# Performance work log

Measured on AMD Instinct MI355X. Metric: run time of the kernel, lower is better.

The kernel has to match this reference:

```python
import jax, jax.numpy as jnp
import numpy as np

B, S, M, D, H, DH = 2, 1024, 1024, 1024, 16, 64
K = S + M                 # key length
R = 2 * K - 1             # relative position table width
EPS = 1e-5


def layer_norm(x, gamma, beta):
    mu = jnp.mean(x, axis=-1, keepdims=True)
    var = jnp.mean(jnp.square(x - mu), axis=-1, keepdims=True)
    return (x - mu) * jax.lax.rsqrt(var + EPS) * gamma + beta


def skew(q_pos, mem_len):
    # q_pos: (B, H, L, R) with R = 2*k_len - 1
    b, h, L, r = q_pos.shape
    pad = jnp.full((b, h, L, 1), -jnp.inf, q_pos.dtype)
    x = jnp.concatenate([q_pos, pad], axis=-1).reshape(b, h, L * (r + 1))
    x = x[..., : L * r].reshape(b, h, L, r)
    k_len = (r + 1) // 2
    start = k_len - 1 - mem_len
    return x[..., start : start + k_len]  # (B, H, L, k_len)


def setup_inputs() -> dict:
    key = jax.random.key(0)
    ks = jax.random.split(key, 9)
    hidden = jax.random.normal(ks[0], (B, S, D), jnp.float32)
    memory = jax.random.normal(ks[1], (B, M, D), jnp.float32)
    pos_emb = jax.random.normal(ks[2], (B, R, DH), jnp.float32)
    # causal mask: query i may attend keys j <= i + M ; True = blocked
    mask = jnp.arange(K)[None, :] > (jnp.arange(S)[:, None] + M)
    sc = 1.0 / np.sqrt(D)
    Wq = jax.random.normal(ks[3], (D, H * DH), jnp.float32) * sc
    Wk = jax.random.normal(ks[4], (D, H * DH), jnp.float32) * sc
    Wv = jax.random.normal(ks[5], (D, H * DH), jnp.float32) * sc
    Wo = jax.random.normal(ks[6], (H * DH, D), jnp.float32) * sc
    gamma = jnp.ones((D,), jnp.float32)
    beta = jnp.zeros((D,), jnp.float32)
    return {"hidden": hidden, "pos_emb": pos_emb, "memory": memory,
            "mask": mask, "Wq": Wq, "Wk": Wk, "Wv": Wv, "Wo": Wo,
            "gamma": gamma, "beta": beta}


def reference(hidden, pos_emb, memory, mask, Wq, Wk, Wv, Wo, gamma, beta):
    mem_len = memory.shape[1]
    combined = jnp.concatenate([memory, hidden], axis=1)  # (B, K, D)
    h_ln = layer_norm(hidden, gamma, beta)                # pre-LN
    c_ln = layer_norm(combined, gamma, beta)
    q = (h_ln @ Wq).reshape(B, S, H, DH).transpose(0, 2, 1, 3)  # (B,H,S,DH)
    k = (c_ln @ Wk).reshape(B, K, H, DH).transpose(0, 2, 1, 3)  # (B,H,K,DH)
    v = (c_ln @ Wv).reshape(B, K, H, DH).transpose(0, 2, 1, 3)
    score = jnp.einsum('bhsd,bhkd->bhsk', q, k)                  # (B,H,S,K)
    q_pos = jnp.einsum('bhsd,brd->bhsr', q, pos_emb)             # (B,H,S,R)
    score = (score + skew(q_pos, mem_len)) * (1.0 / np.sqrt(D))
    score = jnp.where(mask[None, None], -jnp.inf, score)
    p = jax.nn.softmax(score, axis=-1)
    attn = jnp.einsum('bhsk,bhkd->bshd', p, v).reshape(B, S, H * DH)
    out = attn @ Wo
    return h_ln + out
```

## Files before the change

### kernel.cpp

```cpp
#include <hip/hip_runtime.h>
#include <hip/hip_bf16.h>

#define B_ 2
#define S_ 1024
#define M_ 1024
#define D_ 1024
#define H_ 16
#define DH_ 64
#define K_ 2048
#define R_ 4095

#define NEG_BIG (-1e30f)

typedef unsigned short u16;
typedef short short8 __attribute__((ext_vector_type(8)));
typedef float f32x4 __attribute__((ext_vector_type(4)));

__device__ __forceinline__ u16 f2bf(float f) {
  __hip_bfloat16 h = __float2bfloat16(f);
  return *reinterpret_cast<u16*>(&h);
}
__device__ __forceinline__ float bf2f(u16 u) {
  __hip_bfloat16 h;
  *reinterpret_cast<u16*>(&h) = u;
  return __bfloat162float(h);
}

__device__ __forceinline__ void gll16(const void* g, const void* l) {
  __builtin_amdgcn_global_load_lds(
      (const __attribute__((address_space(1))) unsigned int*)g,
      (__attribute__((address_space(3))) unsigned int*)l, 16, 0, 0);
}

__device__ __forceinline__ f32x4 mfma16(short8 a, short8 b, f32x4 c) {
  return __builtin_amdgcn_mfma_f32_16x16x32_bf16(a, b, c, 0, 0, 0);
}

__global__ __launch_bounds__(256) void prep_kernel(
    const float* __restrict__ hidden, const float* __restrict__ memory,
    const float* __restrict__ gamma, const float* __restrict__ beta,
    u16* __restrict__ cln,
    const float* __restrict__ W0, const float* __restrict__ W1,
    const float* __restrict__ W2, const float* __restrict__ W3,
    u16* __restrict__ O0, u16* __restrict__ O1,
    u16* __restrict__ O2, u16* __restrict__ O3,
    const float* __restrict__ pos, u16* __restrict__ posb) {
  __shared__ u16 tile[64][66];
  __shared__ float red[8];
  const int bx = blockIdx.x;
  const int t = threadIdx.x;

  if (bx < 4096) {
    const int b = bx >> 11;
    const int idx = bx & (K_ - 1);
    const float* src = (idx < M_)
        ? memory + (size_t)(b * M_ + idx) * D_
        : hidden + (size_t)(b * S_ + (idx - M_)) * D_;
    const int lane = t & 63, w = t >> 6;
    float4 rv = ((const float4*)src)[t];
    float s = rv.x + rv.y + rv.z + rv.w;
    float ss = rv.x * rv.x + rv.y * rv.y + rv.z * rv.z + rv.w * rv.w;
#pragma unroll
    for (int m = 1; m < 64; m <<= 1) {
      s += __shfl_xor(s, m, 64);
      ss += __shfl_xor(ss, m, 64);
    }
    if (lane == 0) { red[w] = s; red[4 + w] = ss; }
    __syncthreads();
    s = red[0] + red[1] + red[2] + red[3];
    ss = red[4] + red[5] + red[6] + red[7];
    const float mu = s * (1.0f / D_);
    const float var = ss * (1.0f / D_) - mu * mu;
    const float rstd = rsqrtf(var + 1e-5f);
    float4 gv = ((const float4*)gamma)[t];
    float4 bv = ((const float4*)beta)[t];
    ushort4 ov;
    ov.x = f2bf((rv.x - mu) * rstd * gv.x + bv.x);
    ov.y = f2bf((rv.y - mu) * rstd * gv.y + bv.y);
    ov.z = f2bf((rv.z - mu) * rstd * gv.z + bv.z);
    ov.w = f2bf((rv.w - mu) * rstd * gv.w + bv.w);
    ((ushort4*)(cln + (size_t)bx * D_))[t] = ov;
    return;
  }
  if (bx < 5120) {
    const int z = (bx - 4096) >> 8;
    const int rem = (bx - 4096) & 255;
    const float* in; u16* out;
    switch (z) {
      case 0:  in = W0; out = O0; break;
      case 1:  in = W1; out = O1; break;
      case 2:  in = W2; out = O2; break;
      default: in = W3; out = O3; break;
    }
    const int tx = t & 63, ty = t >> 6;
    const int k0 = (rem & 15) * 64, n0 = (rem >> 4) * 64;
#pragma unroll
    for (int i = ty; i < 64; i += 4)
      tile[i][tx] = f2bf(in[(size_t)(k0 + i) * D_ + n0 + tx]);
    __syncthreads();
#pragma unroll
    for (int i = ty; i < 64; i += 4)
      out[(size_t)(n0 + i) * D_ + k0 + tx] = tile[tx][i];
    return;
  }
  const int i = (bx - 5120) * 256 + t;
  const int n4 = B_ * R_ * 64 / 4;
  if (i < n4) {
    float4 v = ((const float4*)pos)[i];
    ushort4 o;
    o.x = f2bf(v.x); o.y = f2bf(v.y); o.z = f2bf(v.z); o.w = f2bf(v.w);
    ((ushort4*)posb)[i] = o;
  }
}

__device__ __forceinline__ int maprow_hidden(int r) {
  return r + ((r >> 10) << 10) + M_;
}

__global__ __launch_bounds__(256, 2) void gemm_bt_kernel(
    const u16* __restrict__ A, const u16* __restrict__ Bt,
    u16* __restrict__ qb, u16* __restrict__ kb, u16* __restrict__ vbT,
    float* __restrict__ Cf, const u16* __restrict__ resid,
    int Kdim, int a_map, int resid_map, int qkv) {
  __shared__ __align__(16) u16 As[128 * 32];
  __shared__ __align__(16) u16 Bs[128 * 32];
  const int t = threadIdx.x;
  const int lane = t & 63, w = t >> 6;
  const int wm = w >> 1, wn = w & 1;
  const int qd = lane >> 4, lr = lane & 15;
  const int m0 = blockIdx.y * 128, n0 = blockIdx.x * 128;

  if (qkv && n0 < 1024 && !(m0 & 1024)) return;

  int ar0 = m0 + (t >> 2), ar1 = ar0 + 64;
  if (a_map) { ar0 = maprow_hidden(ar0); ar1 = maprow_hidden(ar1); }
  const u16* Ag0 = A + (size_t)ar0 * Kdim + (t & 3) * 8;
  const u16* Ag1 = A + (size_t)ar1 * Kdim + (t & 3) * 8;
  const u16* Bg0 = Bt + (size_t)(n0 + (t >> 2)) * Kdim + (t & 3) * 8;
  const u16* Bg1 = Bt + (size_t)(n0 + 64 + (t >> 2)) * Kdim + (t & 3) * 8;

  f32x4 acc[4][4];
#pragma unroll
  for (int mt = 0; mt < 4; mt++)
#pragma unroll
    for (int nt = 0; nt < 4; nt++) acc[mt][nt] = (f32x4){0.f, 0.f, 0.f, 0.f};

  for (int kt = 0; kt < Kdim; kt += 32) {
    gll16(Ag0 + kt, As + w * 512);
    gll16(Ag1 + kt, As + 2048 + w * 512);
    gll16(Bg0 + kt, Bs + w * 512);
    gll16(Bg1 + kt, Bs + 2048 + w * 512);
    __syncthreads();
    short8 af[4], bfr[4];
#pragma unroll
    for (int mt = 0; mt < 4; mt++)
      af[mt] = *(const short8*)&As[(wm * 64 + mt * 16 + lr) * 32 + qd * 8];
#pragma unroll
    for (int nt = 0; nt < 4; nt++)
      bfr[nt] = *(const short8*)&Bs[(wn * 64 + nt * 16 + lr) * 32 + qd * 8];
#pragma unroll
    for (int mt = 0; mt < 4; mt++)
#pragma unroll
      for (int nt = 0; nt < 4; nt++)
        acc[mt][nt] = mfma16(af[mt], bfr[nt], acc[mt][nt]);
    __syncthreads();
  }

  if (qkv) {
#pragma unroll
    for (int mt = 0; mt < 4; mt++)
#pragma unroll
      for (int nt = 0; nt < 4; nt++) {
        const int colb = n0 + wn * 64 + nt * 16;
        const int rowb = m0 + wm * 64 + mt * 16 + qd * 4;
        if (colb < 1024) {
          const int qrow = ((rowb >> 11) << 10) | (rowb & 1023);
#pragma unroll
          for (int r = 0; r < 4; r++)
            qb[(size_t)(qrow + r) * 1024 + colb + lr] = f2bf(acc[mt][nt][r] * 0.03125f);
        } else if (colb < 2048) {
          const int key = rowb & (K_ - 1);
          const int bq = rowb >> 11;
#pragma unroll
          for (int r = 0; r < 4; r++)
            kb[(size_t)(bq * K_ + key + r) * 1024 + (colb - 1024) + lr] = f2bf(acc[mt][nt][r]);
        } else {
          const int nn = colb - 2048 + lr;
          const int bh = ((rowb >> 11) << 4) | (nn >> 6);
          const int dh = nn & 63;
          const int key = rowb & (K_ - 1);
          ushort4 pk;
          pk.x = f2bf(acc[mt][nt][0]);
          pk.y = f2bf(acc[mt][nt][1]);
          pk.z = f2bf(acc[mt][nt][2]);
          pk.w = f2bf(acc[mt][nt][3]);
          *(ushort4*)&vbT[((size_t)bh * 64 + dh) * K_ + key] = pk;
        }
      }
    return;
  }

#pragma unroll
  for (int mt = 0; mt < 4; mt++)
#pragma unroll
    for (int nt = 0; nt < 4; nt++)
#pragma unroll
      for (int r = 0; r < 4; r++) {
        const int row = m0 + wm * 64 + mt * 16 + qd * 4 + r;
        const int col = n0 + wn * 64 + nt * 16 + lr;
        float v = acc[mt][nt][r];
        const int rrow = resid_map ? maprow_hidden(row) : row;
        v += bf2f(resid[(size_t)rrow * 1024 + col]);
        Cf[(size_t)row * 1024 + col] = v;
      }
}

__global__ __launch_bounds__(256, 2) void attn_kernel(
    const u16* __restrict__ qb, const u16* __restrict__ kb,
    const u16* __restrict__ vbT, const u16* __restrict__ pos,
    u16* __restrict__ ab) {
  __shared__ __align__(16) u16 Ks[2][64 * 64];
  __shared__ __align__(16) u16 Vt[2][64 * 64];
  __shared__ __align__(16) u16 Ps[192 * 64];
  __shared__ __align__(16) u16 Pt[4][16 * 68];

  const int t = threadIdx.x;
  const int lane = t & 63, w = t >> 6;
  const int qd = lane >> 4, lr = lane & 15;
  const int i0 = blockIdx.x * 64;
  const int h = blockIdx.y;
  const int b = blockIdx.z;

  const int swz = ((t & 7) ^ ((t >> 3) & 7)) * 8;
  const int c0 = (qd ^ (lr & 7)) * 8;
  const int c1 = c0 ^ 32;
  const int base0 = 960 - i0;
  const int row8 = t >> 3;

#pragma unroll
  for (int rd = 0; rd < 2; rd++)
    gll16(qb + (size_t)(b * S_ + i0 + rd * 32 + row8) * 1024 + h * 64 + swz,
          &Ks[1][0] + rd * 2048 + w * 512);
#pragma unroll
  for (int rd = 0; rd < 2; rd++) {
    gll16(kb + (size_t)(b * K_ + rd * 32 + row8) * 1024 + h * 64 + swz,
          &Ks[0][0] + rd * 2048 + w * 512);
    gll16(vbT + (size_t)((b * H_ + h) * 64 + rd * 32 + row8) * K_ + swz,
          &Vt[0][0] + rd * 2048 + w * 512);
  }
#pragma unroll
  for (int rd = 0; rd < 4; rd++)
    gll16(pos + (size_t)(b * R_ + base0 + rd * 32 + row8) * 64 + swz,
          Ps + rd * 2048 + w * 512);
  __syncthreads();
  const short8 aQ0 = *(const short8*)&Ks[1][(w * 16 + lr) * 64 + c0];
  const short8 aQ1 = *(const short8*)&Ks[1][(w * 16 + lr) * 64 + c1];

  f32x4 accO[4];
#pragma unroll
  for (int d = 0; d < 4; d++) accO[d] = (f32x4){0.f, 0.f, 0.f, 0.f};
  float lsum[4];
#pragma unroll
  for (int r = 0; r < 4; r++) lsum[r] = 0.f;

  const int bw0 = 48 - w * 16;
  const int jmax = min(K_, i0 + 64 + M_);
  int sa = 0, sb = 1, sc = 2;
  int cur = 0;

  for (int j0 = 0, tt = 0; j0 < jmax; j0 += 64, tt++) {
    __syncthreads();

    if (j0 + 64 < jmax) {
      const int nxt = cur ^ 1;
#pragma unroll
      for (int rd = 0; rd < 2; rd++) {
        gll16(kb + (size_t)(b * K_ + j0 + 64 + rd * 32 + row8) * 1024 + h * 64 + swz,
              &Ks[nxt][0] + rd * 2048 + w * 512);
        gll16(vbT + (size_t)((b * H_ + h) * 64 + rd * 32 + row8) * K_ + j0 + 64 + swz,
              &Vt[nxt][0] + rd * 2048 + w * 512);
      }
    }
#pragma unroll
    for (int rd = 0; rd < 2; rd++)
      gll16(pos + (size_t)(b * R_ + base0 + 64 * tt + 128 + rd * 32 + row8) * 64 + swz,
            Ps + ((size_t)sc * 64 + rd * 32) * 64 + w * 512);

    f32x4 sqk[4];
#pragma unroll
    for (int kc = 0; kc < 4; kc++) {
      const short8 bK0 = *(const short8*)&Ks[cur][(kc * 16 + lr) * 64 + c0];
      const short8 bK1 = *(const short8*)&Ks[cur][(kc * 16 + lr) * 64 + c1];
      f32x4 z = {0.f, 0.f, 0.f, 0.f};
      z = mfma16(aQ0, bK0, z);
      sqk[kc] = mfma16(aQ1, bK1, z);
    }
    f32x4 zp[5];
#pragma unroll
    for (int pc = 0; pc < 5; pc++) {
      const int xb = bw0 + pc * 16;
      const int slab = (xb >= 64) ? sb : sa;
      const int pb = slab * 64 + (xb & 63);
      const short8 bP0 = *(const short8*)&Ps[(pb + lr) * 64 + c0];
      const short8 bP1 = *(const short8*)&Ps[(pb + lr) * 64 + c1];
      f32x4 z = {0.f, 0.f, 0.f, 0.f};
      z = mfma16(aQ0, bP0, z);
      zp[pc] = mfma16(aQ1, bP1, z);
    }

    const bool tail = (j0 + 63 > i0 + w * 16 + M_);
    float p[4][4];
#pragma unroll
    for (int r = 0; r < 4; r++) {
      const int iL = qd * 4 + r;
      const int d = 15 + lr - iL;
      const int srcl = qd * 16 + (d & 15);
      const bool hi = (d >> 4) & 1;
      float g0 = __shfl(zp[0][r], srcl, 64);
      float g1 = __shfl(zp[1][r], srcl, 64);
      float g2 = __shfl(zp[2][r], srcl, 64);
      float g3 = __shfl(zp[3][r], srcl, 64);
      float g4 = __shfl(zp[4][r], srcl, 64);
      float s0 = sqk[0][r] + (hi ? g1 : g0);
      float s1 = sqk[1][r] + (hi ? g2 : g1);
      float s2 = sqk[2][r] + (hi ? g3 : g2);
      float s3 = sqk[3][r] + (hi ? g4 : g3);
      if (tail) {
        const int key = j0 + lr, lim = i0 + w * 16 + iL + M_;
        if (key      > lim) s0 = NEG_BIG;
        if (key + 16 > lim) s1 = NEG_BIG;
        if (key + 32 > lim) s2 = NEG_BIG;
        if (key + 48 > lim) s3 = NEG_BIG;
      }
      p[0][r] = __expf(s0);
      p[1][r] = __expf(s1);
      p[2][r] = __expf(s2);
      p[3][r] = __expf(s3);
      lsum[r] += p[0][r] + p[1][r] + p[2][r] + p[3][r];
    }

#pragma unroll
    for (int r = 0; r < 4; r++) {
      const int base = (qd * 4 + r) * 68 + lr;
      Pt[w][base +  0] = f2bf(p[0][r]);
      Pt[w][base + 16] = f2bf(p[1][r]);
      Pt[w][base + 32] = f2bf(p[2][r]);
      Pt[w][base + 48] = f2bf(p[3][r]);
    }
    __asm__ volatile("s_waitcnt lgkmcnt(0)" ::: "memory");
    const short8 aP0 = *(const short8*)&Pt[w][lr * 68 + qd * 8];
    const short8 aP1 = *(const short8*)&Pt[w][lr * 68 + 32 + qd * 8];

#pragma unroll
    for (int d2 = 0; d2 < 4; d2++) {
      const short8 bV0 = *(const short8*)&Vt[cur][(d2 * 16 + lr) * 64 + c0];
      const short8 bV1 = *(const short8*)&Vt[cur][(d2 * 16 + lr) * 64 + c1];
      accO[d2] = mfma16(aP0, bV0, accO[d2]);
      accO[d2] = mfma16(aP1, bV1, accO[d2]);
    }

    const int so = sa; sa = sb; sb = sc; sc = so;
    cur ^= 1;
  }

  float inv[4];
#pragma unroll
  for (int r = 0; r < 4; r++) {
#pragma unroll
    for (int msk = 1; msk < 16; msk <<= 1) lsum[r] += __shfl_xor(lsum[r], msk, 64);
    inv[r] = 1.0f / lsum[r];
  }
#pragma unroll
  for (int d2 = 0; d2 < 4; d2++)
#pragma unroll
    for (int r = 0; r < 4; r++) {
      const int iG = i0 + w * 16 + qd * 4 + r;
      ab[(size_t)(b * S_ + iG) * 1024 + h * 64 + d2 * 16 + lr] = f2bf(accO[d2][r] * inv[r]);
    }
}

extern "C" void kernel_launch(void* const* d_in, const int* in_sizes, int n_in,
                              void* d_out, int out_size, void* d_ws, size_t ws_size,
                              hipStream_t stream) {
  const float* hidden = (const float*)d_in[0];
  const float* pos    = (const float*)d_in[1];
  const float* memory = (const float*)d_in[2];
  const float* Wq = (const float*)d_in[4];
  const float* Wk = (const float*)d_in[5];
  const float* Wv = (const float*)d_in[6];
  const float* Wo = (const float*)d_in[7];
  const float* gamma = (const float*)d_in[8];
  const float* beta  = (const float*)d_in[9];

  char* ws = (char*)d_ws;
  u16* cln  = (u16*)(ws);
  u16* qb   = (u16*)(ws + 8388608);
  u16* kb   = (u16*)(ws + 12582912);
  u16* vbT  = (u16*)(ws + 20971520);
  u16* ab   = (u16*)(ws + 29360128);
  u16* WqT  = (u16*)(ws + 33554432);
  u16* WkT  = WqT + 1048576;
  u16* WvT  = WkT + 1048576;
  u16* WoT  = WvT + 1048576;
  u16* posb = (u16*)(ws + 41943040);

  prep_kernel<<<dim3(5632), 256, 0, stream>>>(
      hidden, memory, gamma, beta, cln,
      Wq, Wk, Wv, Wo, WqT, WkT, WvT, WoT, pos, posb);
  gemm_bt_kernel<<<dim3(24, 32), 256, 0, stream>>>(
      cln, WqT, qb, kb, vbT, nullptr, nullptr, 1024, 0, 0, 1);
  attn_kernel<<<dim3(S_ / 64, H_, B_), 256, 0, stream>>>(qb, kb, vbT, posb, ab);
  gemm_bt_kernel<<<dim3(8, 16), 256, 0, stream>>>(
      ab, WoT, nullptr, nullptr, nullptr, (float*)d_out, cln, 1024, 0, 1, 0);
}
```

Before: 223.3 us.

## Fuse all stages into one persistent kernel with grid-wide atomic barriers

Replaces the four launches (prep, QKV GEMM, attention, output GEMM) with a single persistent kernel of 512 blocks that strides over each stage's work items and separates stages with an atomic counter barrier. The output GEMM now uses 128x64 tiles over 256 blocks, and the attention blocks reverse query-tile order for the second batch to balance causal work. The aim is to remove launch gaps and tail effects between stages. In exchange it adds a memset launch, spin-barrier overhead, and relies on all 512 blocks being co-resident, which risks deadlock if occupancy is lower than assumed.

After: 565.9 us. 153% more time.

```diff
diff --git a/kernel.cpp b/kernel.cpp
--- a/kernel.cpp
+++ b/kernel.cpp
@@ -11,6 +11,7 @@
 #define R_ 4095
 
 #define NEG_BIG (-1e30f)
+#define NBLK 512
 
 typedef unsigned short u16;
 typedef short short8 __attribute__((ext_vector_type(8)));
@@ -36,347 +37,385 @@
   return __builtin_amdgcn_mfma_f32_16x16x32_bf16(a, b, c, 0, 0, 0);
 }
 
-__global__ __launch_bounds__(256) void prep_kernel(
-    const float* __restrict__ hidden, const float* __restrict__ memory,
-    const float* __restrict__ gamma, const float* __restrict__ beta,
-    u16* __restrict__ cln,
-    const float* __restrict__ W0, const float* __restrict__ W1,
-    const float* __restrict__ W2, const float* __restrict__ W3,
-    u16* __restrict__ O0, u16* __restrict__ O1,
-    u16* __restrict__ O2, u16* __restrict__ O3,
-    const float* __restrict__ pos, u16* __restrict__ posb) {
-  __shared__ u16 tile[64][66];
-  __shared__ float red[8];
-  const int bx = blockIdx.x;
-  const int t = threadIdx.x;
-
-  if (bx < 4096) {
-    const int b = bx >> 11;
-    const int idx = bx & (K_ - 1);
-    const float* src = (idx < M_)
-        ? memory + (size_t)(b * M_ + idx) * D_
-        : hidden + (size_t)(b * S_ + (idx - M_)) * D_;
-    const int lane = t & 63, w = t >> 6;
-    float4 rv = ((const float4*)src)[t];
-    float s = rv.x + rv.y + rv.z + rv.w;
-    float ss = rv.x * rv.x + rv.y * rv.y + rv.z * rv.z + rv.w * rv.w;
-#pragma unroll
-    for (int m = 1; m < 64; m <<= 1) {
-      s += __shfl_xor(s, m, 64);
-      ss += __shfl_xor(ss, m, 64);
-    }
-    if (lane == 0) { red[w] = s; red[4 + w] = ss; }
-    __syncthreads();
-    s = red[0] + red[1] + red[2] + red[3];
-    ss = red[4] + red[5] + red[6] + red[7];
-    const float mu = s * (1.0f / D_);
-    const float var = ss * (1.0f / D_) - mu * mu;
-    const float rstd = rsqrtf(var + 1e-5f);
-    float4 gv = ((const float4*)gamma)[t];
-    float4 bv = ((const float4*)beta)[t];
-    ushort4 ov;
-    ov.x = f2bf((rv.x - mu) * rstd * gv.x + bv.x);
-    ov.y = f2bf((rv.y - mu) * rstd * gv.y + bv.y);
-    ov.z = f2bf((rv.z - mu) * rstd * gv.z + bv.z);
-    ov.w = f2bf((rv.w - mu) * rstd * gv.w + bv.w);
-    ((ushort4*)(cln + (size_t)bx * D_))[t] = ov;
-    return;
+__device__ __forceinline__ void gbar(unsigned* c, unsigned tgt) {
+  __syncthreads();
+  if (threadIdx.x == 0) {
+    __hip_atomic_fetch_add(c, 1u, __ATOMIC_RELEASE, __HIP_MEMORY_SCOPE_AGENT);
+    while (__hip_atomic_load(c, __ATOMIC_ACQUIRE, __HIP_MEMORY_SCOPE_AGENT) < tgt)
+      __builtin_amdgcn_s_sleep(4);
   }
-  if (bx < 5120) {
-    const int z = (bx - 4096) >> 8;
-    const int rem = (bx - 4096) & 255;
-    const float* in; u16* out;
-    switch (z) {
-      case 0:  in = W0; out = O0; break;
-      case 1:  in = W1; out = O1; break;
-      case 2:  in = W2; out = O2; break;
-      default: in = W3; out = O3; break;
-    }
-    const int tx = t & 63, ty = t >> 6;
-    const int k0 = (rem & 15) * 64, n0 = (rem >> 4) * 64;
-#pragma unroll
-    for (int i = ty; i < 64; i += 4)
-      tile[i][tx] = f2bf(in[(size_t)(k0 + i) * D_ + n0 + tx]);
-    __syncthreads();
-#pragma unroll
-    for (int i = ty; i < 64; i += 4)
-      out[(size_t)(n0 + i) * D_ + k0 + tx] = tile[tx][i];
-    return;
-  }
-  const int i = (bx - 5120) * 256 + t;
-  const int n4 = B_ * R_ * 64 / 4;
-  if (i < n4) {
-    float4 v = ((const float4*)pos)[i];
-    ushort4 o;
-    o.x = f2bf(v.x); o.y = f2bf(v.y); o.z = f2bf(v.z); o.w = f2bf(v.w);
-    ((ushort4*)posb)[i] = o;
-  }
+  __syncthreads();
 }
 
 __device__ __forceinline__ int maprow_hidden(int r) {
   return r + ((r >> 10) << 10) + M_;
 }
 
-__global__ __launch_bounds__(256, 2) void gemm_bt_kernel(
-    const u16* __restrict__ A, const u16* __restrict__ Bt,
-    u16* __restrict__ qb, u16* __restrict__ kb, u16* __restrict__ vbT,
-    float* __restrict__ Cf, const u16* __restrict__ resid,
-    int Kdim, int a_map, int resid_map, int qkv) {
-  __shared__ __align__(16) u16 As[128 * 32];
-  __shared__ __align__(16) u16 Bs[128 * 32];
-  const int t = threadIdx.x;
-  const int lane = t & 63, w = t >> 6;
-  const int wm = w >> 1, wn = w & 1;
-  const int qd = lane >> 4, lr = lane & 15;
-  const int m0 = blockIdx.y * 128, n0 = blockIdx.x * 128;
-
-  if (qkv && n0 < 1024 && !(m0 & 1024)) return;
-
-  int ar0 = m0 + (t >> 2), ar1 = ar0 + 64;
-  if (a_map) { ar0 = maprow_hidden(ar0); ar1 = maprow_hidden(ar1); }
-  const u16* Ag0 = A + (size_t)ar0 * Kdim + (t & 3) * 8;
-  const u16* Ag1 = A + (size_t)ar1 * Kdim + (t & 3) * 8;
-  const u16* Bg0 = Bt + (size_t)(n0 + (t >> 2)) * Kdim + (t & 3) * 8;
-  const u16* Bg1 = Bt + (size_t)(n0 + 64 + (t >> 2)) * Kdim + (t & 3) * 8;
-
-  f32x4 acc[4][4];
-#pragma unroll
-  for (int mt = 0; mt < 4; mt++)
-#pragma unroll
-    for (int nt = 0; nt < 4; nt++) acc[mt][nt] = (f32x4){0.f, 0.f, 0.f, 0.f};
-
-  for (int kt = 0; kt < Kdim; kt += 32) {
-    gll16(Ag0 + kt, As + w * 512);
-    gll16(Ag1 + kt, As + 2048 + w * 512);
-    gll16(Bg0 + kt, Bs + w * 512);
-    gll16(Bg1 + kt, Bs + 2048 + w * 512);
-    __syncthreads();
-    short8 af[4], bfr[4];
-#pragma unroll
-    for (int mt = 0; mt < 4; mt++)
-      af[mt] = *(const short8*)&As[(wm * 64 + mt * 16 + lr) * 32 + qd * 8];
-#pragma unroll
-    for (int nt = 0; nt < 4; nt++)
-      bfr[nt] = *(const short8*)&Bs[(wn * 64 + nt * 16 + lr) * 32 + qd * 8];
-#pragma unroll
-    for (int mt = 0; mt < 4; mt++)
-#pragma unroll
-      for (int nt = 0; nt < 4; nt++)
-        acc[mt][nt] = mfma16(af[mt], bfr[nt], acc[mt][nt]);
-    __syncthreads();
-  }
-
-  if (qkv) {
-#pragma unroll
-    for (int mt = 0; mt < 4; mt++)
-#pragma unroll
-      for (int nt = 0; nt < 4; nt++) {
-        const int colb = n0 + wn * 64 + nt * 16;
-        const int rowb = m0 + wm * 64 + mt * 16 + qd * 4;
-        if (colb < 1024) {
-          const int qrow = ((rowb >> 11) << 10) | (rowb & 1023);
-#pragma unroll
-          for (int r = 0; r < 4; r++)
-            qb[(size_t)(qrow + r) * 1024 + colb + lr] = f2bf(acc[mt][nt][r] * 0.03125f);
-        } else if (colb < 2048) {
-          const int key = rowb & (K_ - 1);
-          const int bq = rowb >> 11;
-#pragma unroll
-          for (int r = 0; r < 4; r++)
-            kb[(size_t)(bq * K_ + key + r) * 1024 + (colb - 1024) + lr] = f2bf(acc[mt][nt][r]);
-        } else {
-          const int nn = colb - 2048 + lr;
-          const int bh = ((rowb >> 11) << 4) | (nn >> 6);
-          const int dh = nn & 63;
-          const int key = rowb & (K_ - 1);
-          ushort4 pk;
-          pk.x = f2bf(acc[mt][nt][0]);
-          pk.y = f2bf(acc[mt][nt][1]);
-          pk.z = f2bf(acc[mt][nt][2]);
-          pk.w = f2bf(acc[mt][nt][3]);
-          *(ushort4*)&vbT[((size_t)bh * 64 + dh) * K_ + key] = pk;
-        }
-      }
-    return;
-  }
-
-#pragma unroll
-  for (int mt = 0; mt < 4; mt++)
-#pragma unroll
-    for (int nt = 0; nt < 4; nt++)
-#pragma unroll
-      for (int r = 0; r < 4; r++) {
-        const int row = m0 + wm * 64 + mt * 16 + qd * 4 + r;
-        const int col = n0 + wn * 64 + nt * 16 + lr;
-        float v = acc[mt][nt][r];
-        const int rrow = resid_map ? maprow_hidden(row) : row;
-        v += bf2f(resid[(size_t)rrow * 1024 + col]);
-        Cf[(size_t)row * 1024 + col] = v;
-      }
-}
-
-__global__ __launch_bounds__(256, 2) void attn_kernel(
-    const u16* __restrict__ qb, const u16* __restrict__ kb,
-    const u16* __restrict__ vbT, const u16* __restrict__ pos,
-    u16* __restrict__ ab) {
-  __shared__ __align__(16) u16 Ks[2][64 * 64];
-  __shared__ __align__(16) u16 Vt[2][64 * 64];
-  __shared__ __align__(16) u16 Ps[192 * 64];
-  __shared__ __align__(16) u16 Pt[4][16 * 68];
-
+__global__ __launch_bounds__(256, 2) void fused_kernel(
+    const float* __restrict__ hidden, const float* __restrict__ posf,
+    const float* __restrict__ memory,
+    const float* __restrict__ Wq, const float* __restrict__ Wk,
+    const float* __restrict__ Wv, const float* __restrict__ Wo,
+    const float* __restrict__ gamma, const float* __restrict__ beta,
+    u16* __restrict__ cln, u16* __restrict__ qb, u16* __restrict__ kb,
+    u16* __restrict__ vbT, u16* __restrict__ ab,
+    u16* __restrict__ WqT, u16* __restrict__ posb,
+    float* __restrict__ outp, unsigned* __restrict__ bar) {
+  __shared__ __align__(16) u16 smem[33024];
+  const int bid = blockIdx.x;
   const int t = threadIdx.x;
   const int lane = t & 63, w = t >> 6;
   const int qd = lane >> 4, lr = lane & 15;
-  const int i0 = blockIdx.x * 64;
-  const int h = blockIdx.y;
-  const int b = blockIdx.z;
-
-  const int swz = ((t & 7) ^ ((t >> 3) & 7)) * 8;
-  const int c0 = (qd ^ (lr & 7)) * 8;
-  const int c1 = c0 ^ 32;
-  const int base0 = 960 - i0;
-  const int row8 = t >> 3;
-
-#pragma unroll
-  for (int rd = 0; rd < 2; rd++)
-    gll16(qb + (size_t)(b * S_ + i0 + rd * 32 + row8) * 1024 + h * 64 + swz,
-          &Ks[1][0] + rd * 2048 + w * 512);
-#pragma unroll
-  for (int rd = 0; rd < 2; rd++) {
-    gll16(kb + (size_t)(b * K_ + rd * 32 + row8) * 1024 + h * 64 + swz,
-          &Ks[0][0] + rd * 2048 + w * 512);
-    gll16(vbT + (size_t)((b * H_ + h) * 64 + rd * 32 + row8) * K_ + swz,
-          &Vt[0][0] + rd * 2048 + w * 512);
+
+  for (int wk = bid; wk < 5632; wk += NBLK) {
+    __syncthreads();
+    if (wk < 4096) {
+      float* red = (float*)smem;
+      const int b = wk >> 11;
+      const int idx = wk & (K_ - 1);
+      const float* src = (idx < M_)
+          ? memory + (size_t)(b * M_ + idx) * D_
+          : hidden + (size_t)(b * S_ + (idx - M_)) * D_;
+      float4 rv = ((const float4*)src)[t];
+      float s = rv.x + rv.y + rv.z + rv.w;
+      float ss = rv.x * rv.x + rv.y * rv.y + rv.z * rv.z + rv.w * rv.w;
+#pragma unroll
+      for (int m = 1; m < 64; m <<= 1) {
+        s += __shfl_xor(s, m, 64);
+        ss += __shfl_xor(ss, m, 64);
+      }
+      if (lane == 0) { red[w] = s; red[4 + w] = ss; }
+      __syncthreads();
+      s = red[0] + red[1] + red[2] + red[3];
+      ss = red[4] + red[5] + red[6] + red[7];
+      const float mu = s * (1.0f / D_);
+      const float var = ss * (1.0f / D_) - mu * mu;
+      const float rstd = rsqrtf(var + 1e-5f);
+      float4 gv = ((const float4*)gamma)[t];
+      float4 bv = ((const float4*)beta)[t];
+      ushort4 ov;
+      ov.x = f2bf((rv.x - mu) * rstd * gv.x + bv.x);
+      ov.y = f2bf((rv.y - mu) * rstd * gv.y + bv.y);
+      ov.z = f2bf((rv.z - mu) * rstd * gv.z + bv.z);
+      ov.w = f2bf((rv.w - mu) * rstd * gv.w + bv.w);
+      ((ushort4*)(cln + (size_t)wk * D_))[t] = ov;
+    } else if (wk < 5120) {
+      u16 (*tile)[66] = (u16(*)[66])smem;
+      const int z = (wk - 4096) >> 8;
+      const int rem = (wk - 4096) & 255;
+      const float* in; u16* out;
+      switch (z) {
+        case 0:  in = Wq; out = WqT;              break;
+        case 1:  in = Wk; out = WqT + 1048576;    break;
+        case 2:  in = Wv; out = WqT + 2097152;    break;
+        default: in = Wo; out = WqT + 3145728;    break;
+      }
+      const int tx = t & 63, ty = t >> 6;
+      const int k0 = (rem & 15) * 64, n0 = (rem >> 4) * 64;
+#pragma unroll
+      for (int i = ty; i < 64; i += 4)
+        tile[i][tx] = f2bf(in[(size_t)(k0 + i) * D_ + n0 + tx]);
+      __syncthreads();
+#pragma unroll
+      for (int i = ty; i < 64; i += 4)
+        out[(size_t)(n0 + i) * D_ + k0 + tx] = tile[tx][i];
+    } else {
+      const int i = (wk - 5120) * 256 + t;
+      const int n4 = B_ * R_ * 64 / 4;
+      if (i < n4) {
+        float4 v = ((const float4*)posf)[i];
+        ushort4 o;
+        o.x = f2bf(v.x); o.y = f2bf(v.y); o.z = f2bf(v.z); o.w = f2bf(v.w);
+        ((ushort4*)posb)[i] = o;
+      }
+    }
   }
-#pragma unroll
-  for (int rd = 0; rd < 4; rd++)
-    gll16(pos + (size_t)(b * R_ + base0 + rd * 32 + row8) * 64 + swz,
-          Ps + rd * 2048 + w * 512);
-  __syncthreads();
-  const short8 aQ0 = *(const short8*)&Ks[1][(w * 16 + lr) * 64 + c0];
-  const short8 aQ1 = *(const short8*)&Ks[1][(w * 16 + lr) * 64 + c1];
-
-  f32x4 accO[4];
-#pragma unroll
-  for (int d = 0; d < 4; d++) accO[d] = (f32x4){0.f, 0.f, 0.f, 0.f};
-  float lsum[4];
-#pragma unroll
-  for (int r = 0; r < 4; r++) lsum[r] = 0.f;
-
-  const int bw0 = 48 - w * 16;
-  const int jmax = min(K_, i0 + 64 + M_);
-  int sa = 0, sb = 1, sc = 2;
-  int cur = 0;
-
-  for (int j0 = 0, tt = 0; j0 < jmax; j0 += 64, tt++) {
+  gbar(bar, NBLK);
+
+  {
+    u16* As = smem;
+    u16* Bs = smem + 4096;
+    const int wm = w >> 1, wn = w & 1;
+    for (int tl = bid; tl < 768; tl += NBLK) {
+      const int bx = tl % 24, by = tl / 24;
+      const int m0 = by * 128, n0 = bx * 128;
+      if (n0 < 1024 && !(m0 & 1024)) continue;
+
+      const u16* Ag0 = cln + (size_t)(m0 + (t >> 2)) * 1024 + (t & 3) * 8;
+      const u16* Ag1 = Ag0 + (size_t)64 * 1024;
+      const u16* Bg0 = WqT + (size_t)(n0 + (t >> 2)) * 1024 + (t & 3) * 8;
+      const u16* Bg1 = Bg0 + (size_t)64 * 1024;
+
+      f32x4 acc[4][4];
+#pragma unroll
+      for (int mt = 0; mt < 4; mt++)
+#pragma unroll
+        for (int nt = 0; nt < 4; nt++) acc[mt][nt] = (f32x4){0.f, 0.f, 0.f, 0.f};
+
+      for (int kt = 0; kt < 1024; kt += 32) {
+        gll16(Ag0 + kt, As + w * 512);
+        gll16(Ag1 + kt, As + 2048 + w * 512);
+        gll16(Bg0 + kt, Bs + w * 512);
+        gll16(Bg1 + kt, Bs + 2048 + w * 512);
+        __syncthreads();
+        short8 af[4], bfr[4];
+#pragma unroll
+        for (int mt = 0; mt < 4; mt++)
+          af[mt] = *(const short8*)&As[(wm * 64 + mt * 16 + lr) * 32 + qd * 8];
+#pragma unroll
+        for (int nt = 0; nt < 4; nt++)
+          bfr[nt] = *(const short8*)&Bs[(wn * 64 + nt * 16 + lr) * 32 + qd * 8];
+#pragma unroll
+        for (int mt = 0; mt < 4; mt++)
+#pragma unroll
+          for (int nt = 0; nt < 4; nt++)
+            acc[mt][nt] = mfma16(af[mt], bfr[nt], acc[mt][nt]);
+        __syncthreads();
+      }
+
+#pragma unroll
+      for (int mt = 0; mt < 4; mt++)
+#pragma unroll
+        for (int nt = 0; nt < 4; nt++) {
+          const int colb = n0 + wn * 64 + nt * 16;
+          const int rowb = m0 + wm * 64 + mt * 16 + qd * 4;
+          if (colb < 1024) {
+            const int qrow = ((rowb >> 11) << 10) | (rowb & 1023);
+#pragma unroll
+            for (int r = 0; r < 4; r++)
+              qb[(size_t)(qrow + r) * 1024 + colb + lr] = f2bf(acc[mt][nt][r] * 0.03125f);
+          } else if (colb < 2048) {
+            const int key = rowb & (K_ - 1);
+            const int bq = rowb >> 11;
+#pragma unroll
+            for (int r = 0; r < 4; r++)
+              kb[(size_t)(bq * K_ + key + r) * 1024 + (colb - 1024) + lr] = f2bf(acc[mt][nt][r]);
+          } else {
+            const int nn = colb - 2048 + lr;
+            const int bh = ((rowb >> 11) << 4) | (nn >> 6);
+            const int dh = nn & 63;
+            const int key = rowb & (K_ - 1);
+            ushort4 pk;
+            pk.x = f2bf(acc[mt][nt][0]);
+            pk.y = f2bf(acc[mt][nt][1]);
+            pk.z = f2bf(acc[mt][nt][2]);
+            pk.w = f2bf(acc[mt][nt][3]);
+            *(ushort4*)&vbT[((size_t)bh * 64 + dh) * K_ + key] = pk;
+          }
+        }
+    }
+  }
+  gbar(bar, 2 * NBLK);
+
+  {
+    int qt = bid & 15;
+    const int h = (bid >> 4) & 15;
+    const int b = bid >> 8;
+    if (b) qt = 15 - qt;
+    const int i0 = qt * 64;
+
+    u16* KsB = smem;
+    u16* VtB = smem + 8192;
+    u16* PsB = smem + 16384;
+    u16* PtW = smem + 28672 + w * 1088;
+
+    const int swz = ((t & 7) ^ ((t >> 3) & 7)) * 8;
+    const int c0 = (qd ^ (lr & 7)) * 8;
+    const int c1 = c0 ^ 32;
+    const int base0 = 960 - i0;
+    const int row8 = t >> 3;
+
+#pragma unroll
+    for (int rd = 0; rd < 2; rd++)
+      gll16(qb + (size_t)(b * S_ + i0 + rd * 32 + row8) * 1024 + h * 64 + swz,
+            KsB + 4096 + rd * 2048 + w * 512);
+#pragma unroll
+    for (int rd = 0; rd < 2; rd++) {
+      gll16(kb + (size_t)(b * K_ + rd * 32 + row8) * 1024 + h * 64 + swz,
+            KsB + rd * 2048 + w * 512);
+      gll16(vbT + (size_t)((b * H_ + h) * 64 + rd * 32 + row8) * K_ + swz,
+            VtB + rd * 2048 + w * 512);
+    }
+#pragma unroll
+    for (int rd = 0; rd < 4; rd++)
+      gll16(posb + (size_t)(b * R_ + base0 + rd * 32 + row8) * 64 + swz,
+            PsB + rd * 2048 + w * 512);
     __syncthreads();
-
-    if (j0 + 64 < jmax) {
-      const int nxt = cur ^ 1;
-#pragma unroll
-      for (int rd = 0; rd < 2; rd++) {
-        gll16(kb + (size_t)(b * K_ + j0 + 64 + rd * 32 + row8) * 1024 + h * 64 + swz,
-              &Ks[nxt][0] + rd * 2048 + w * 512);
-        gll16(vbT + (size_t)((b * H_ + h) * 64 + rd * 32 + row8) * K_ + j0 + 64 + swz,
-              &Vt[nxt][0] + rd * 2048 + w * 512);
-      }
-    }
-#pragma unroll
-    for (int rd = 0; rd < 2; rd++)
-      gll16(pos + (size_t)(b * R_ + base0 + 64 * tt + 128 + rd * 32 + row8) * 64 + swz,
-            Ps + ((size_t)sc * 64 + rd * 32) * 64 + w * 512);
-
-    f32x4 sqk[4];
-#pragma unroll
-    for (int kc = 0; kc < 4; kc++) {
-      const short8 bK0 = *(const short8*)&Ks[cur][(kc * 16 + lr) * 64 + c0];
-      const short8 bK1 = *(const short8*)&Ks[cur][(kc * 16 + lr) * 64 + c1];
-      f32x4 z = {0.f, 0.f, 0.f, 0.f};
-      z = mfma16(aQ0, bK0, z);
-      sqk[kc] = mfma16(aQ1, bK1, z);
-    }
-    f32x4 zp[5];
-#pragma unroll
-    for (int pc = 0; pc < 5; pc++) {
-      const int xb = bw0 + pc * 16;
-      const int slab = (xb >= 64) ? sb : sa;
-      const int pb = slab * 64 + (xb & 63);
-      const short8 bP0 = *(const short8*)&Ps[(pb + lr) * 64 + c0];
-      const short8 bP1 = *(const short8*)&Ps[(pb + lr) * 64 + c1];
-      f32x4 z = {0.f, 0.f, 0.f, 0.f};
-      z = mfma16(aQ0, bP0, z);
-      zp[pc] = mfma16(aQ1, bP1, z);
-    }
-
-    const bool tail = (j0 + 63 > i0 + w * 16 + M_);
-    float p[4][4];
+    const short8 aQ0 = *(const short8*)&KsB[4096 + (w * 16 + lr) * 64 + c0];
+    const short8 aQ1 = *(const short8*)&KsB[4096 + (w * 16 + lr) * 64 + c1];
+
+    f32x4 accO[4];
+#pragma unroll
+    for (int d = 0; d < 4; d++) accO[d] = (f32x4){0.f, 0.f, 0.f, 0.f};
+    float lsum[4];
+#pragma unroll
+    for (int r = 0; r < 4; r++) lsum[r] = 0.f;
+
+    const int bw0 = 48 - w * 16;
+    const int jmax = min(K_, i0 + 64 + M_);
+    int sa = 0, sb = 1, sc = 2;
+    int cur = 0;
+
+    for (int j0 = 0, tt = 0; j0 < jmax; j0 += 64, tt++) {
+      __syncthreads();
+      if (j0 + 64 < jmax) {
+        const int nxt = cur ^ 1;
+#pragma unroll
+        for (int rd = 0; rd < 2; rd++) {
+          gll16(kb + (size_t)(b * K_ + j0 + 64 + rd * 32 + row8) * 1024 + h * 64 + swz,
+                KsB + (nxt << 12) + rd * 2048 + w * 512);
+          gll16(vbT + (size_t)((b * H_ + h) * 64 + rd * 32 + row8) * K_ + j0 + 64 + swz,
+                VtB + (nxt << 12) + rd * 2048 + w * 512);
+        }
+      }
+#pragma unroll
+      for (int rd = 0; rd < 2; rd++)
+        gll16(posb + (size_t)(b * R_ + base0 + 64 * tt + 128 + rd * 32 + row8) * 64 + swz,
+              PsB + (sc * 64 + rd * 32) * 64 + w * 512);
+
+      f32x4 sqk[4];
+#pragma unroll
+      for (int kc = 0; kc < 4; kc++) {
+        const short8 bK0 = *(const short8*)&KsB[(cur << 12) + (kc * 16 + lr) * 64 + c0];
+        const short8 bK1 = *(const short8*)&KsB[(cur << 12) + (kc * 16 + lr) * 64 + c1];
+        f32x4 z = {0.f, 0.f, 0.f, 0.f};
+        z = mfma16(aQ0, bK0, z);
+        sqk[kc] = mfma16(aQ1, bK1, z);
+      }
+      f32x4 zp[5];
+#pragma unroll
+      for (int pc = 0; pc < 5; pc++) {
+        const int xb = bw0 + pc * 16;
+        const int slab = (xb >= 64) ? sb : sa;
+        const int pb = slab * 64 + (xb & 63);
+        const short8 bP0 = *(const short8*)&PsB[(pb + lr) * 64 + c0];
+        const short8 bP1 = *(const short8*)&PsB[(pb + lr) * 64 + c1];
+        f32x4 z = {0.f, 0.f, 0.f, 0.f};
+        z = mfma16(aQ0, bP0, z);
+        zp[pc] = mfma16(aQ1, bP1, z);
+      }
+
+      const bool tail = (j0 + 63 > i0 + w * 16 + M_);
+      float p[4][4];
+#pragma unroll
+      for (int r = 0; r < 4; r++) {
+        const int iL = qd * 4 + r;
+        const int d = 15 + lr - iL;
+        const int srcl = qd * 16 + (d & 15);
+        const bool hi = (d >> 4) & 1;
+        float g0 = __shfl(zp[0][r], srcl, 64);
+        float g1 = __shfl(zp[1][r], srcl, 64);
+        float g2 = __shfl(zp[2][r], srcl, 64);
+        float g3 = __shfl(zp[3][r], srcl, 64);
+        float g4 = __shfl(zp[4][r], srcl, 64);
+        float s0 = sqk[0][r] + (hi ? g1 : g0);
+        float s1 = sqk[1][r] + (hi ? g2 : g1);
+        float s2 = sqk[2][r] + (hi ? g3 : g2);
+        float s3 = sqk[3][r] + (hi ? g4 : g3);
+        if (tail) {
+          const int key = j0 + lr, lim = i0 + w * 16 + iL + M_;
+          if (key      > lim) s0 = NEG_BIG;
+          if (key + 16 > lim) s1 = NEG_BIG;
+          if (key + 32 > lim) s2 = NEG_BIG;
+          if (key + 48 > lim) s3 = NEG_BIG;
+        }
+        p[0][r] = __expf(s0);
+        p[1][r] = __expf(s1);
+        p[2][r] = __expf(s2);
+        p[3][r] = __expf(s3);
+        lsum[r] += p[0][r] + p[1][r] + p[2][r] + p[3][r];
+      }
+
+#pragma unroll
+      for (int r = 0; r < 4; r++) {
+        const int base = (qd * 4 + r) * 68 + lr;
+        PtW[base +  0] = f2bf(p[0][r]);
+        PtW[base + 16] = f2bf(p[1][r]);
+        PtW[base + 32] = f2bf(p[2][r]);
+        PtW[base + 48] = f2bf(p[3][r]);
+      }
+      __asm__ volatile("s_waitcnt lgkmcnt(0)" ::: "memory");
+      const short8 aP0 = *(const short8*)&PtW[lr * 68 + qd * 8];
+      const short8 aP1 = *(const short8*)&PtW[lr * 68 + 32 + qd * 8];
+
+#pragma unroll
+      for (int d2 = 0; d2 < 4; d2++) {
+        const short8 bV0 = *(const short8*)&VtB[(cur << 12) + (d2 * 16 + lr) * 64 + c0];
+        const short8 bV1 = *(const short8*)&VtB[(cur << 12) + (d2 * 16 + lr) * 64 + c1];
+        accO[d2] = mfma16(aP0, bV0, accO[d2]);
+        accO[d2] = mfma16(aP1, bV1, accO[d2]);
+      }
+
+      const int so = sa; sa = sb; sb = sc; sc = so;
+      cur ^= 1;
+    }
+
+    float inv[4];
 #pragma unroll
     for (int r = 0; r < 4; r++) {
-      const int iL = qd * 4 + r;
-      const int d = 15 + lr - iL;
-      const int srcl = qd * 16 + (d & 15);
-      const bool hi = (d >> 4) & 1;
-      float g0 = __shfl(zp[0][r], srcl, 64);
-      float g1 = __shfl(zp[1][r], srcl, 64);
-      float g2 = __shfl(zp[2][r], srcl, 64);
-      float g3 = __shfl(zp[3][r], srcl, 64);
-      float g4 = __shfl(zp[4][r], srcl, 64);
-      float s0 = sqk[0][r] + (hi ? g1 : g0);
-      float s1 = sqk[1][r] + (hi ? g2 : g1);
-      float s2 = sqk[2][r] + (hi ? g3 : g2);
-      float s3 = sqk[3][r] + (hi ? g4 : g3);
-      if (tail) {
-        const int key = j0 + lr, lim = i0 + w * 16 + iL + M_;
-        if (key      > lim) s0 = NEG_BIG;
-        if (key + 16 > lim) s1 = NEG_BIG;
-        if (key + 32 > lim) s2 = NEG_BIG;
-        if (key + 48 > lim) s3 = NEG_BIG;
-      }
-      p[0][r] = __expf(s0);
-      p[1][r] = __expf(s1);
-      p[2][r] = __expf(s2);
-      p[3][r] = __expf(s3);
-      lsum[r] += p[0][r] + p[1][r] + p[2][r] + p[3][r];
-    }
-
-#pragma unroll
-    for (int r = 0; r < 4; r++) {
-      const int base = (qd * 4 + r) * 68 + lr;
-      Pt[w][base +  0] = f2bf(p[0][r]);
-      Pt[w][base + 16] = f2bf(p[1][r]);
-      Pt[w][base + 32] = f2bf(p[2][r]);
-      Pt[w][base + 48] = f2bf(p[3][r]);
-    }
-    __asm__ volatile("s_waitcnt lgkmcnt(0)" ::: "memory");
-    const short8 aP0 = *(const short8*)&Pt[w][lr * 68 + qd * 8];
-    const short8 aP1 = *(const short8*)&Pt[w][lr * 68 + 32 + qd * 8];
-
-#pragma unroll
-    for (int d2 = 0; d2 < 4; d2++) {
-      const short8 bV0 = *(const short8*)&Vt[cur][(d2 * 16 + lr) * 64 + c0];
-      const short8 bV1 = *(const short8*)&Vt[cur][(d2 * 16 + lr) * 64 + c1];
-      accO[d2] = mfma16(aP0, bV0, accO[d2]);
-      accO[d2] = mfma16(aP1, bV1, accO[d2]);
-    }
-
-    const int so = sa; sa = sb; sb = sc; sc = so;
-    cur ^= 1;
+#pragma unroll
+      for (int msk = 1; msk < 16; msk <<= 1) lsum[r] += __shfl_xor(lsum[r], msk, 64);
+      inv[r] = 1.0f / lsum[r];
+    }
+#pragma unroll
+    for (int d2 = 0; d2 < 4; d2++)
+#pragma unroll
+      for (int r = 0; r < 4; r++) {
+        const int iG = i0 + w * 16 + qd * 4 + r;
+        ab[(size_t)(b * S_ + iG) * 1024 + h * 64 + d2 * 16 + lr] = f2bf(accO[d2][r] * inv[r]);
+      }
   }
-
-  float inv[4];
-#pragma unroll
-  for (int r = 0; r < 4; r++) {
-#pragma unroll
-    for (int msk = 1; msk < 16; msk <<= 1) lsum[r] += __shfl_xor(lsum[r], msk, 64);
-    inv[r] = 1.0f / lsum[r];
+  gbar(bar, 3 * NBLK);
+
+  if (bid < 256) {
+    u16* As = smem;
+    u16* Bs = smem + 4096;
+    const int wm = w >> 1, wn = w & 1;
+    const int m0 = (bid >> 4) * 128, n0 = (bid & 15) * 64;
+    const u16* WoT = WqT + 3145728;
+
+    const u16* Ag0 = ab + (size_t)(m0 + (t >> 2)) * 1024 + (t & 3) * 8;
+    const u16* Ag1 = Ag0 + (size_t)64 * 1024;
+    const u16* Bg0 = WoT + (size_t)(n0 + (t >> 2)) * 1024 + (t & 3) * 8;
+
+    f32x4 acc[4][2];
+#pragma unroll
+    for (int mt = 0; mt < 4; mt++)
+#pragma unroll
+      for (int nt = 0; nt < 2; nt++) acc[mt][nt] = (f32x4){0.f, 0.f, 0.f, 0.f};
+
+    for (int kt = 0; kt < 1024; kt += 32) {
+      gll16(Ag0 + kt, As + w * 512);
+      gll16(Ag1 + kt, As + 2048 + w * 512);
+      gll16(Bg0 + kt, Bs + w * 512);
+      __syncthreads();
+      short8 af[4], bfr[2];
+#pragma unroll
+      for (int mt = 0; mt < 4; mt++)
+        af[mt] = *(const short8*)&As[(wm * 64 + mt * 16 + lr) * 32 + qd * 8];
+#pragma unroll
+      for (int nt = 0; nt < 2; nt++)
+        bfr[nt] = *(const short8*)&Bs[(wn * 32 + nt * 16 + lr) * 32 + qd * 8];
+#pragma unroll
+      for (int mt = 0; mt < 4; mt++)
+#pragma unroll
+        for (int nt = 0; nt < 2; nt++)
+          acc[mt][nt] = mfma16(af[mt], bfr[nt], acc[mt][nt]);
+      __syncthreads();
+    }
+
+#pragma unroll
+    for (int mt = 0; mt < 4; mt++)
+#pragma unroll
+      for (int nt = 0; nt < 2; nt++)
+#pragma unroll
+        for (int r = 0; r < 4; r++) {
+          const int row = m0 + wm * 64 + mt * 16 + qd * 4 + r;
+          const int col = n0 + wn * 32 + nt * 16 + lr;
+          float v = acc[mt][nt][r] + bf2f(cln[(size_t)maprow_hidden(row) * 1024 + col]);
+          outp[(size_t)row * 1024 + col] = v;
+        }
   }
-#pragma unroll
-  for (int d2 = 0; d2 < 4; d2++)
-#pragma unroll
-    for (int r = 0; r < 4; r++) {
-      const int iG = i0 + w * 16 + qd * 4 + r;
-      ab[(size_t)(b * S_ + iG) * 1024 + h * 64 + d2 * 16 + lr] = f2bf(accO[d2][r] * inv[r]);
-    }
 }
 
 extern "C" void kernel_launch(void* const* d_in, const int* in_sizes, int n_in,
@@ -399,17 +438,11 @@
   u16* vbT  = (u16*)(ws + 20971520);
   u16* ab   = (u16*)(ws + 29360128);
   u16* WqT  = (u16*)(ws + 33554432);
-  u16* WkT  = WqT + 1048576;
-  u16* WvT  = WkT + 1048576;
-  u16* WoT  = WvT + 1048576;
   u16* posb = (u16*)(ws + 41943040);
-
-  prep_kernel<<<dim3(5632), 256, 0, stream>>>(
-      hidden, memory, gamma, beta, cln,
-      Wq, Wk, Wv, Wo, WqT, WkT, WvT, WoT, pos, posb);
-  gemm_bt_kernel<<<dim3(24, 32), 256, 0, stream>>>(
-      cln, WqT, qb, kb, vbT, nullptr, nullptr, 1024, 0, 0, 1);
-  attn_kernel<<<dim3(S_ / 64, H_, B_), 256, 0, stream>>>(qb, kb, vbT, posb, ab);
-  gemm_bt_kernel<<<dim3(8, 16), 256, 0, stream>>>(
-      ab, WoT, nullptr, nullptr, nullptr, (float*)d_out, cln, 1024, 0, 1, 0);
-}
+  unsigned* bar = (unsigned*)(ws + 42991360);
+
+  hipMemsetAsync(bar, 0, sizeof(unsigned), stream);
+  fused_kernel<<<dim3(NBLK), 256, 0, stream>>>(
+      hidden, pos, memory, Wq, Wk, Wv, Wo, gamma, beta,
+      cln, qb, kb, vbT, ab, WqT, posb, (float*)d_out, bar);
+}
```
